# Performance work log

Measured on AMD Instinct MI355X. Metric: run time of the kernel, lower is better.

The kernel has to match this reference:

```python
import jax, jax.numpy as jnp
import numpy as np

N = 20000
E = 640000
D = 128
NORM_FACTOR = 100.0
LN_EPS = 1e-5


def _layer_norm(x, g, b):
    mu = jnp.mean(x, axis=-1, keepdims=True)
    var = jnp.var(x, axis=-1, keepdims=True)
    return (x - mu) * jax.lax.rsqrt(var + LN_EPS) * g + b


def setup_inputs() -> dict:
    key = jax.random.key(0)
    ks = jax.random.split(key, 16)

    def lin(k, fan_in, shape):
        bound = 1.0 / np.sqrt(fan_in)
        return jax.random.uniform(k, shape, jnp.float32, -bound, bound)

    h = jax.random.normal(ks[0], (N, D), jnp.float32)
    distances = jax.random.uniform(ks[1], (E, 1), jnp.float32)
    edges = jax.random.randint(ks[2], (2, E), 0, N, jnp.int64)
    node_mask = jnp.ones((N, 1), jnp.float32)
    edge_mask = jnp.ones((E, 1), jnp.float32)

    return {
        "h": h, "distances": distances, "node_mask": node_mask, "edge_mask": edge_mask,
        # linear: in->out
        "lin_w": lin(ks[3], D, (D, D)), "lin_b": lin(ks[4], D, (D,)),
        # att_mlp: (2D+1)->2D -> 2D->D -> D->1
        "att_w1": lin(ks[5], 2 * D + 1, (2 * D, 2 * D + 1)), "att_b1": lin(ks[5], 2 * D + 1, (2 * D,)),
        "att_w2": lin(ks[6], 2 * D, (D, 2 * D)), "att_b2": lin(ks[6], 2 * D, (D,)),
        "att_w3": lin(ks[7], D, (1, D)), "att_b3": lin(ks[7], D, (1,)),
        # node_mlp: D->D, LN, SiLU, D->D
        "nm_w1": lin(ks[8], D, (D, D)), "nm_b1": lin(ks[8], D, (D,)),
        "nm_ln_g": jnp.ones((D,), jnp.float32), "nm_ln_b": jnp.zeros((D,), jnp.float32),
        "nm_w2": lin(ks[9], D, (D, D)), "nm_b2": lin(ks[9], D, (D,)),
        # final LayerNorm
        "ln_g": jnp.ones((D,), jnp.float32), "ln_b": jnp.zeros((D,), jnp.float32),
        "edges": edges,
    }


def reference(h, distances, node_mask, edge_mask,
              lin_w, lin_b, att_w1, att_b1, att_w2, att_b2, att_w3, att_b3,
              nm_w1, nm_b1, nm_ln_g, nm_ln_b, nm_w2, nm_b2, ln_g, ln_b, edges):
    x = h @ lin_w.T + lin_b                                  # [N, D]
    row, col = edges[0], edges[1]
    x_row = x[row]                                           # [E, D]
    x_col = x[col]                                           # [E, D]

    # DenseAtt
    d = distances * edge_mask
    x_cat = jnp.concatenate([x_row, x_col, d], axis=1)       # [E, 2D+1]
    a = jax.nn.silu(x_cat @ att_w1.T + att_b1)
    a = jax.nn.silu(a @ att_w2.T + att_b2)
    att = jax.nn.sigmoid(a @ att_w3.T + att_b3) * edge_mask  # [E, 1]

    agg = x_col * att                                        # [E, D]
    out = jax.ops.segment_sum(agg, row, num_segments=N) / NORM_FACTOR

    # node_mlp + residual
    o = out @ nm_w1.T + nm_b1
    o = jax.nn.silu(_layer_norm(o, nm_ln_g, nm_ln_b))
    o = o @ nm_w2.T + nm_b2
    hh = o + x

    hh = _layer_norm(hh, ln_g, ln_b)
    hh = jax.nn.silu(hh)                                     # act = SiLU
    return hh
```

## Files before the change

### kernel.cpp

```cpp
#include <hip/hip_runtime.h>
#include <hip/hip_bf16.h>

#define N_NODES 20000
#define E_EDGES 640000
#define DIM 128
#define CAP 96
#define EPB 64
#define NPB 8
#define XST 264

typedef __attribute__((ext_vector_type(8))) short bf16x8;
typedef __attribute__((ext_vector_type(4))) float f32x4;

#define LOG2E 1.44269504f
__device__ __forceinline__ float fsilu(float x) {
    return x * __builtin_amdgcn_rcpf(1.f + __builtin_amdgcn_exp2f(-LOG2E * x));
}
__device__ __forceinline__ float fsig(float x) {
    return __builtin_amdgcn_rcpf(1.f + __builtin_amdgcn_exp2f(-LOG2E * x));
}

__device__ __forceinline__ unsigned short f2bf(float x) {
    union { float f; unsigned u; } v; v.f = x;
    unsigned r = (v.u + 0x7fffu + ((v.u >> 16) & 1u)) >> 16;
    return (unsigned short)r;
}
__device__ __forceinline__ float bf2f(unsigned short s) {
    union { unsigned u; float f; } v; v.u = ((unsigned)s) << 16;
    return v.f;
}
__device__ __forceinline__ unsigned pack_bf16(float lo, float hi) {
    union { float f; unsigned u; } a, b; a.f = lo; b.f = hi;
    unsigned ul = a.u + 0x8000u, uh = b.u + 0x8000u;
    return __builtin_amdgcn_perm(uh, ul, 0x07060302u);
}

#define PRE_PREP_BLOCKS 64
#define PRE_LIN_BLOCKS  625
#define PRE_ADJ_BLOCKS  2500
__global__ __launch_bounds__(256) void pre_kernel(
    const float* __restrict__ w1, const float* __restrict__ w2,
    unsigned short* __restrict__ w1b, float* __restrict__ w1last,
    unsigned short* __restrict__ w2b,
    const float* __restrict__ h, const float* __restrict__ lw,
    const float* __restrict__ lb, float* __restrict__ x,
    unsigned short* __restrict__ xb,
    const int* __restrict__ edges, int* __restrict__ cnt,
    int2* __restrict__ adj2, int E) {
    __shared__ float hs[32][128];
    int b = blockIdx.x;
    int t = threadIdx.x;

    if (b < PRE_PREP_BLOCKS) {
        int i = b * 256 + t;
        const int stride = PRE_PREP_BLOCKS * 256;
        for (int idx = i; idx < 256 * 256; idx += stride) {
            int o = idx >> 8, k = idx & 255;
            w1b[idx] = f2bf(w1[o * 257 + k]);
        }
        for (int idx = i; idx < 128 * 256; idx += stride) {
            int n2 = idx >> 8, p = idx & 255;
            int bb = p & ~31, off = p & 31;
            int ksrc = bb + (off >> 1) + ((off & 1) << 4);
            w2b[idx] = f2bf(w2[n2 * 256 + ksrc]);
        }
        for (int idx = i; idx < 256; idx += stride)
            w1last[idx] = w1[idx * 257 + 256];
    } else if (b < PRE_PREP_BLOCKS + PRE_LIN_BLOCKS) {
        int nb = b - PRE_PREP_BLOCKS;
        int n0 = nb * 32;
        int ch = t & 127, g = t >> 7;
#pragma unroll
        for (int j = 0; j < 16; ++j) hs[g * 16 + j][ch] = h[(size_t)(n0 + g * 16 + j) * DIM + ch];
        __syncthreads();
        float acc[16];
#pragma unroll
        for (int j = 0; j < 16; ++j) acc[j] = 0.f;
        for (int kc = 0; kc < 128; kc += 4) {
            float4 wv = *(const float4*)&lw[(size_t)ch * DIM + kc];
#pragma unroll
            for (int j = 0; j < 16; ++j)
                acc[j] += wv.x * hs[g * 16 + j][kc] + wv.y * hs[g * 16 + j][kc + 1]
                        + wv.z * hs[g * 16 + j][kc + 2] + wv.w * hs[g * 16 + j][kc + 3];
        }
        float bias = lb[ch];
#pragma unroll
        for (int j = 0; j < 16; ++j) {
            float v = acc[j] + bias;
            int n = n0 + g * 16 + j;
            x[(size_t)n * DIM + ch] = v;
            xb[(size_t)n * DIM + ch] = f2bf(v);
        }
    } else {
        int e = (b - PRE_PREP_BLOCKS - PRE_LIN_BLOCKS) * 256 + t;
        if (e < E) {
            int r = edges[e];
            int col = edges[E + e];
            int slot = atomicAdd(&cnt[r], 1);
            if (slot < CAP) { int2 v; v.x = e; v.y = col; adj2[(size_t)r * CAP + slot] = v; }
        }
    }
}

__global__ __launch_bounds__(512, 4) void edge_kernel(
    const unsigned short* __restrict__ xb,
    const float* __restrict__ dist, const float* __restrict__ emask,
    const int* __restrict__ edges,
    const unsigned short* __restrict__ w1b, const float* __restrict__ w1last,
    const float* __restrict__ b1,
    const unsigned short* __restrict__ w2b, const float* __restrict__ b2,
    const float* __restrict__ w3, const float* __restrict__ b3v,
    float* __restrict__ att, int E) {
    __shared__ unsigned short buf[EPB * XST];
    __shared__ float part[8][EPB];
    __shared__ float dvals[EPB];
    __shared__ int ridx[EPB], cidx[EPB];

    int tid = threadIdx.x;
    int eb = blockIdx.x * EPB;

    if (tid < EPB) {
        int e = eb + tid;
        ridx[tid] = edges[e];
        cidx[tid] = edges[E + e];
        dvals[tid] = dist[e] * emask[e];
    }
    __syncthreads();

#pragma unroll
    for (int i = 0; i < 4; ++i) {
        int c = tid + 512 * i;
        int r = c >> 5;
        int cb = (c & 31) * 8;
        const unsigned short* src;
        if (cb < 128) src = xb + (size_t)ridx[r] * DIM + cb;
        else          src = xb + (size_t)cidx[r] * DIM + (cb - 128);
        *(bf16x8*)&buf[r * XST + cb] = *(const bf16x8*)src;
    }

    int wave = tid >> 6, lane = tid & 63;
    int lrow = lane & 15, quad = lane >> 4;
    int nb = wave * 32;

    float bias0 = b1[nb + lrow], bias1 = b1[nb + 16 + lrow];
    float wl0 = w1last[nb + lrow], wl1 = w1last[nb + 16 + lrow];
    int n2 = wave * 16 + lrow;
    float bias2 = b2[n2];
    float w3v = w3[n2];

    __syncthreads();

    f32x4 z = {0.f, 0.f, 0.f, 0.f};
    f32x4 acc1[4][2];
#pragma unroll
    for (int mt = 0; mt < 4; ++mt)
#pragma unroll
        for (int nt = 0; nt < 2; ++nt) acc1[mt][nt] = z;

    for (int kk = 0; kk < 8; ++kk) {
        int ka = kk * 32 + quad * 8;
        bf16x8 a[4];
#pragma unroll
        for (int mt = 0; mt < 4; ++mt)
            a[mt] = *(bf16x8*)&buf[(mt * 16 + lrow) * XST + ka];
#pragma unroll
        for (int nt = 0; nt < 2; ++nt) {
            int n = nb + nt * 16 + lrow;
            bf16x8 bfrag = *(const bf16x8*)&w1b[(size_t)n * 256 + ka];
#pragma unroll
            for (int mt = 0; mt < 4; ++mt)
                acc1[mt][nt] = __builtin_amdgcn_mfma_f32_16x16x32_bf16(a[mt], bfrag, acc1[mt][nt], 0, 0, 0);
        }
    }
    __syncthreads();

    int colbase = nb + 2 * lrow;
#pragma unroll
    for (int mt = 0; mt < 4; ++mt) {
#pragma unroll
        for (int r = 0; r < 4; ++r) {
            int m = mt * 16 + quad * 4 + r;
            float dv = dvals[m];
            float v0 = fsilu(acc1[mt][0][r] + bias0 + dv * wl0);
            float v1 = fsilu(acc1[mt][1][r] + bias1 + dv * wl1);
            *(unsigned*)&buf[m * XST + colbase] = pack_bf16(v0, v1);
        }
    }
    __syncthreads();

    f32x4 acc2[4];
#pragma unroll
    for (int mt = 0; mt < 4; ++mt) acc2[mt] = z;

    for (int kk = 0; kk < 8; ++kk) {
        int ka = kk * 32 + quad * 8;
        bf16x8 bfrag = *(const bf16x8*)&w2b[(size_t)n2 * 256 + ka];
#pragma unroll
        for (int mt = 0; mt < 4; ++mt) {
            bf16x8 a = *(bf16x8*)&buf[(mt * 16 + lrow) * XST + ka];
            acc2[mt] = __builtin_amdgcn_mfma_f32_16x16x32_bf16(a, bfrag, acc2[mt], 0, 0, 0);
        }
    }

    float s[4][4];
#pragma unroll
    for (int mt = 0; mt < 4; ++mt)
#pragma unroll
        for (int r = 0; r < 4; ++r)
            s[mt][r] = fsilu(acc2[mt][r] + bias2) * w3v;
#pragma unroll
    for (int off = 1; off < 16; off <<= 1) {
#pragma unroll
        for (int mt = 0; mt < 4; ++mt)
#pragma unroll
            for (int r = 0; r < 4; ++r)
                s[mt][r] += __shfl_xor(s[mt][r], off);
    }
    if (lrow == 0) {
#pragma unroll
        for (int mt = 0; mt < 4; ++mt)
#pragma unroll
            for (int r = 0; r < 4; ++r)
                part[wave][mt * 16 + quad * 4 + r] = s[mt][r];
    }
    __syncthreads();

    if (tid < EPB) {
        float ssum = b3v[0];
#pragma unroll
        for (int w = 0; w < 8; ++w) ssum += part[w][tid];
        att[eb + tid] = fsig(ssum) * emask[eb + tid];
    }
}

__global__ __launch_bounds__(256) void node_kernel(
    const float* __restrict__ attv, const int2* __restrict__ adj2, const int* __restrict__ cnt,
    const unsigned short* __restrict__ xb,
    const float* __restrict__ x,
    const float* __restrict__ w1, const float* __restrict__ bb1,
    const float* __restrict__ lng, const float* __restrict__ lnb,
    const float* __restrict__ w2, const float* __restrict__ bb2,
    const float* __restrict__ gF, const float* __restrict__ bF,
    float* __restrict__ out, int E) {
    __shared__ float atts[NPB][CAP];
    __shared__ int   cols[NPB][CAP];
    __shared__ float outv[NPB][128];
    __shared__ float bufs[NPB][128];
    __shared__ float mu_s[NPB], rs_s[NPB];
    __shared__ int cnts[NPB];

    int t = threadIdx.x;
    int n0 = blockIdx.x * NPB;

    if (t < NPB) { int c = cnt[n0 + t]; cnts[t] = c > CAP ? CAP : c; }
    __syncthreads();

    {
        int jg = t >> 5, l = t & 31;
        int c = cnts[jg];
        const int2* al = adj2 + (size_t)(n0 + jg) * CAP;
        for (int i = l; i < c; i += 32) {
            int2 v = al[i];
            atts[jg][i] = attv[v.x];
            cols[jg][i] = v.y;
        }
    }
    __syncthreads();

    int w = t >> 6, lane = t & 63;
#pragma unroll
    for (int jj = 0; jj < 2; ++jj) {
        int j = w * 2 + jj;
        int c = cnts[j];
        float lo0 = 0.f, hi0 = 0.f, lo1 = 0.f, hi1 = 0.f;
        float lo2 = 0.f, hi2 = 0.f, lo3 = 0.f, hi3 = 0.f;
        int i = 0;
        for (; i + 3 < c; i += 4) {
            unsigned u0 = *(const unsigned*)&xb[(size_t)cols[j][i]     * DIM + lane * 2];
            unsigned u1 = *(const unsigned*)&xb[(size_t)cols[j][i + 1] * DIM + lane * 2];
            unsigned u2 = *(const unsigned*)&xb[(size_t)cols[j][i + 2] * DIM + lane * 2];
            unsigned u3 = *(const unsigned*)&xb[(size_t)cols[j][i + 3] * DIM + lane * 2];
            float w0 = atts[j][i], w1v = atts[j][i + 1], w2v = atts[j][i + 2], w3v = atts[j][i + 3];
            lo0 += w0 * bf2f((unsigned short)(u0 & 0xffff)); hi0 += w0 * bf2f((unsigned short)(u0 >> 16));
            lo1 += w1v * bf2f((unsigned short)(u1 & 0xffff)); hi1 += w1v * bf2f((unsigned short)(u1 >> 16));
            lo2 += w2v * bf2f((unsigned short)(u2 & 0xffff)); hi2 += w2v * bf2f((unsigned short)(u2 >> 16));
            lo3 += w3v * bf2f((unsigned short)(u3 & 0xffff)); hi3 += w3v * bf2f((unsigned short)(u3 >> 16));
        }
        for (; i < c; ++i) {
            unsigned u0 = *(const unsigned*)&xb[(size_t)cols[j][i] * DIM + lane * 2];
            float w0 = atts[j][i];
            lo0 += w0 * bf2f((unsigned short)(u0 & 0xffff));
            hi0 += w0 * bf2f((unsigned short)(u0 >> 16));
        }
        outv[j][lane * 2]     = ((lo0 + lo1) + (lo2 + lo3)) * 0.01f;
        outv[j][lane * 2 + 1] = ((hi0 + hi1) + (hi2 + hi3)) * 0.01f;
    }
    __syncthreads();

    int h = t >> 7, ch = t & 127;
    float xres[4];
#pragma unroll
    for (int jj = 0; jj < 4; ++jj)
        xres[jj] = x[(size_t)(n0 + h * 4 + jj) * DIM + ch];

    float a1[4] = {0, 0, 0, 0};
    for (int kc = 0; kc < 128; kc += 4) {
        float4 wv = *(const float4*)&w1[(size_t)ch * DIM + kc];
#pragma unroll
        for (int jj = 0; jj < 4; ++jj) {
            int j = h * 4 + jj;
            a1[jj] += wv.x * outv[j][kc] + wv.y * outv[j][kc + 1] + wv.z * outv[j][kc + 2] + wv.w * outv[j][kc + 3];
        }
    }
    float bias1 = bb1[ch];
#pragma unroll
    for (int jj = 0; jj < 4; ++jj) bufs[h * 4 + jj][ch] = a1[jj] + bias1;
    __syncthreads();

    {
        int j = t >> 5, l = t & 31;
        float s = 0.f, qq = 0.f;
#pragma unroll
        for (int i = 0; i < 4; ++i) { float v = bufs[j][l + 32 * i]; s += v; qq += v * v; }
#pragma unroll
        for (int off = 16; off; off >>= 1) { s += __shfl_xor(s, off); qq += __shfl_xor(qq, off); }
        if (l == 0) {
            float mu = s * (1.f / 128.f);
            float var = qq * (1.f / 128.f) - mu * mu;
            mu_s[j] = mu; rs_s[j] = __builtin_amdgcn_rsqf(var + 1e-5f);
        }
    }
    __syncthreads();

    float g = lng[ch], bb = lnb[ch];
    float h2[4];
#pragma unroll
    for (int jj = 0; jj < 4; ++jj) {
        int j = h * 4 + jj;
        h2[jj] = fsilu((bufs[j][ch] - mu_s[j]) * rs_s[j] * g + bb);
    }
    __syncthreads();
#pragma unroll
    for (int jj = 0; jj < 4; ++jj) bufs[h * 4 + jj][ch] = h2[jj];
    __syncthreads();

    float a3[4] = {0, 0, 0, 0};
    for (int kc = 0; kc < 128; kc += 4) {
        float4 wv = *(const float4*)&w2[(size_t)ch * DIM + kc];
#pragma unroll
        for (int jj = 0; jj < 4; ++jj) {
            int j = h * 4 + jj;
            a3[jj] += wv.x * bufs[j][kc] + wv.y * bufs[j][kc + 1] + wv.z * bufs[j][kc + 2] + wv.w * bufs[j][kc + 3];
        }
    }
    float bias2 = bb2[ch];
    float hh[4];
#pragma unroll
    for (int jj = 0; jj < 4; ++jj) hh[jj] = a3[jj] + bias2 + xres[jj];
    __syncthreads();
#pragma unroll
    for (int jj = 0; jj < 4; ++jj) bufs[h * 4 + jj][ch] = hh[jj];
    __syncthreads();

    {
        int j = t >> 5, l = t & 31;
        float s = 0.f, qq = 0.f;
#pragma unroll
        for (int i = 0; i < 4; ++i) { float v = bufs[j][l + 32 * i]; s += v; qq += v * v; }
#pragma unroll
        for (int off = 16; off; off >>= 1) { s += __shfl_xor(s, off); qq += __shfl_xor(qq, off); }
        if (l == 0) {
            float mu = s * (1.f / 128.f);
            float var = qq * (1.f / 128.f) - mu * mu;
            mu_s[j] = mu; rs_s[j] = __builtin_amdgcn_rsqf(var + 1e-5f);
        }
    }
    __syncthreads();

    float gf = gF[ch], bf = bF[ch];
#pragma unroll
    for (int jj = 0; jj < 4; ++jj) {
        int j = h * 4 + jj;
        float y = (hh[jj] - mu_s[j]) * rs_s[j] * gf + bf;
        out[(size_t)(n0 + j) * DIM + ch] = fsilu(y);
    }
}

extern "C" void kernel_launch(void* const* d_in, const int* in_sizes, int n_in,
                              void* d_out, int out_size, void* d_ws, size_t ws_size,
                              hipStream_t stream) {
    const float* h         = (const float*)d_in[0];
    const float* distances = (const float*)d_in[1];
    const float* edge_mask = (const float*)d_in[3];
    const float* lin_w     = (const float*)d_in[4];
    const float* lin_b     = (const float*)d_in[5];
    const float* att_w1    = (const float*)d_in[6];
    const float* att_b1    = (const float*)d_in[7];
    const float* att_w2    = (const float*)d_in[8];
    const float* att_b2    = (const float*)d_in[9];
    const float* att_w3    = (const float*)d_in[10];
    const float* att_b3    = (const float*)d_in[11];
    const float* nm_w1     = (const float*)d_in[12];
    const float* nm_b1     = (const float*)d_in[13];
    const float* nm_ln_g   = (const float*)d_in[14];
    const float* nm_ln_b   = (const float*)d_in[15];
    const float* nm_w2     = (const float*)d_in[16];
    const float* nm_b2     = (const float*)d_in[17];
    const float* ln_g      = (const float*)d_in[18];
    const float* ln_b      = (const float*)d_in[19];
    const int*   edges     = (const int*)d_in[20];
    float* out = (float*)d_out;

    const int N = N_NODES, E = E_EDGES;

    char* ws = (char*)d_ws;
    float* x            = (float*)ws;            ws += (size_t)N * DIM * 4;
    unsigned short* xb  = (unsigned short*)ws;   ws += (size_t)N * DIM * 2;
    float* attv         = (float*)ws;            ws += (size_t)E * 4;
    int* cnt            = (int*)ws;              ws += (size_t)N * 4;
    int2* adj2          = (int2*)ws;             ws += (size_t)N * CAP * 8;
    unsigned short* w1b = (unsigned short*)ws;   ws += 256 * 256 * 2;
    float* w1last       = (float*)ws;            ws += 256 * 4;
    unsigned short* w2b = (unsigned short*)ws;   ws += 128 * 256 * 2;

    hipMemsetAsync(cnt, 0, (size_t)N * 4, stream);

    pre_kernel<<<PRE_PREP_BLOCKS + PRE_LIN_BLOCKS + PRE_ADJ_BLOCKS, 256, 0, stream>>>(
        att_w1, att_w2, w1b, w1last, w2b,
        h, lin_w, lin_b, x, xb,
        edges, cnt, adj2, E);
    edge_kernel<<<E / EPB, 512, 0, stream>>>(xb, distances, edge_mask, edges,
                                             w1b, w1last, att_b1, w2b, att_b2,
                                             att_w3, att_b3, attv, E);
    node_kernel<<<N / NPB, 256, 0, stream>>>(attv, adj2, cnt, xb, x,
                                             nm_w1, nm_b1, nm_ln_g, nm_ln_b,
                                             nm_w2, nm_b2, ln_g, ln_b, out, E);
}
```

Before: 490.7 us.

## Precompute per-node first attention layer projections instead of per-edge GEMM

Splits the first attention MLP layer W1·[x_row,x_col,d] into per-node projections P_row=W1a·x+b1 and P_col=W1b·x, computed once per node in a new kernel. The edge kernel then gathers the two 256-wide bf16 projection rows per edge, adds them plus the distance term, and applies SiLU, removing the largest per-edge MFMA GEMM. This trades E×256×256 FLOPs for N×256×256 plus twice-as-wide gathers (512 bf16 values per edge instead of 256). It adds an extra bf16 rounding of the projections before summation and extra workspace.

```diff
diff --git a/kernel.cpp b/kernel.cpp
--- a/kernel.cpp
+++ b/kernel.cpp
@@ -40,7 +40,7 @@
 #define PRE_ADJ_BLOCKS  2500
 __global__ __launch_bounds__(256) void pre_kernel(
     const float* __restrict__ w1, const float* __restrict__ w2,
-    unsigned short* __restrict__ w1b, float* __restrict__ w1last,
+    unsigned short* __restrict__ w1b, float* __restrict__ w1p,
     unsigned short* __restrict__ w2b,
     const float* __restrict__ h, const float* __restrict__ lw,
     const float* __restrict__ lb, float* __restrict__ x,
@@ -64,8 +64,11 @@
             int ksrc = bb + (off >> 1) + ((off & 1) << 4);
             w2b[idx] = f2bf(w2[n2 * 256 + ksrc]);
         }
-        for (int idx = i; idx < 256; idx += stride)
-            w1last[idx] = w1[idx * 257 + 256];
+        for (int idx = i; idx < 256; idx += stride) {
+            int bb = idx & ~31, off = idx & 31;
+            int ksrc = bb + (off >> 1) + ((off & 1) << 4);
+            w1p[idx] = w1[ksrc * 257 + 256];
+        }
     } else if (b < PRE_PREP_BLOCKS + PRE_LIN_BLOCKS) {
         int nb = b - PRE_PREP_BLOCKS;
         int n0 = nb * 32;
@@ -102,17 +105,53 @@
     }
 }
 
+#define PRC_NPB 16
+__global__ __launch_bounds__(256) void prc_kernel(
+    const unsigned short* __restrict__ xb,
+    const unsigned short* __restrict__ w1b,
+    const float* __restrict__ b1,
+    unsigned short* __restrict__ pr, unsigned short* __restrict__ pc) {
+    int n0 = blockIdx.x * PRC_NPB;
+    int w = threadIdx.x >> 6, lane = threadIdx.x & 63;
+    int lrow = lane & 15, quad = lane >> 4;
+
+    bf16x8 a[4];
+#pragma unroll
+    for (int kk = 0; kk < 4; ++kk)
+        a[kk] = *(const bf16x8*)&xb[(size_t)(n0 + lrow) * DIM + kk * 32 + quad * 8];
+
+    f32x4 z = {0.f, 0.f, 0.f, 0.f};
+#pragma unroll
+    for (int i = 0; i < 8; ++i) {
+        int gt = w * 8 + i;
+        int half = gt >> 4;
+        int obase = (gt & 15) * 16;
+        f32x4 acc = z;
+#pragma unroll
+        for (int kk = 0; kk < 4; ++kk) {
+            bf16x8 bfrag = *(const bf16x8*)&w1b[(size_t)(obase + lrow) * 256 + half * 128 + kk * 32 + quad * 8];
+            acc = __builtin_amdgcn_mfma_f32_16x16x32_bf16(a[kk], bfrag, acc, 0, 0, 0);
+        }
+        int o = obase + lrow;
+        float bias = half ? 0.f : b1[o];
+        unsigned short* dst = half ? pc : pr;
+#pragma unroll
+        for (int r = 0; r < 4; ++r)
+            dst[(size_t)(n0 + quad * 4 + r) * 256 + o] = f2bf(acc[r] + bias);
+    }
+}
+
 __global__ __launch_bounds__(512, 4) void edge_kernel(
-    const unsigned short* __restrict__ xb,
+    const unsigned short* __restrict__ pr, const unsigned short* __restrict__ pc,
     const float* __restrict__ dist, const float* __restrict__ emask,
     const int* __restrict__ edges,
-    const unsigned short* __restrict__ w1b, const float* __restrict__ w1last,
-    const float* __restrict__ b1,
+    const float* __restrict__ w1p,
     const unsigned short* __restrict__ w2b, const float* __restrict__ b2,
     const float* __restrict__ w3, const float* __restrict__ b3v,
     float* __restrict__ att, int E) {
     __shared__ unsigned short buf[EPB * XST];
     __shared__ float part[8][EPB];
+    __shared__ float w1ps[256];
     __shared__ float dvals[EPB];
     __shared__ int ridx[EPB], cidx[EPB];
 
@@ -125,72 +164,51 @@
         cidx[tid] = edges[E + e];
         dvals[tid] = dist[e] * emask[e];
     }
-    __syncthreads();
-
-#pragma unroll
-    for (int i = 0; i < 4; ++i) {
-        int c = tid + 512 * i;
-        int r = c >> 5;
-        int cb = (c & 31) * 8;
-        const unsigned short* src;
-        if (cb < 128) src = xb + (size_t)ridx[r] * DIM + cb;
-        else          src = xb + (size_t)cidx[r] * DIM + (cb - 128);
-        *(bf16x8*)&buf[r * XST + cb] = *(const bf16x8*)src;
-    }
+    if (tid >= 64 && tid < 320) w1ps[tid - 64] = w1p[tid - 64];
 
     int wave = tid >> 6, lane = tid & 63;
     int lrow = lane & 15, quad = lane >> 4;
-    int nb = wave * 32;
-
-    float bias0 = b1[nb + lrow], bias1 = b1[nb + 16 + lrow];
-    float wl0 = w1last[nb + lrow], wl1 = w1last[nb + 16 + lrow];
     int n2 = wave * 16 + lrow;
     float bias2 = b2[n2];
     float w3v = w3[n2];
 
     __syncthreads();
 
-    f32x4 z = {0.f, 0.f, 0.f, 0.f};
-    f32x4 acc1[4][2];
-#pragma unroll
-    for (int mt = 0; mt < 4; ++mt)
-#pragma unroll
-        for (int nt = 0; nt < 2; ++nt) acc1[mt][nt] = z;
-
-    for (int kk = 0; kk < 8; ++kk) {
-        int ka = kk * 32 + quad * 8;
-        bf16x8 a[4];
-#pragma unroll
-        for (int mt = 0; mt < 4; ++mt)
-            a[mt] = *(bf16x8*)&buf[(mt * 16 + lrow) * XST + ka];
-#pragma unroll
-        for (int nt = 0; nt < 2; ++nt) {
-            int n = nb + nt * 16 + lrow;
-            bf16x8 bfrag = *(const bf16x8*)&w1b[(size_t)n * 256 + ka];
-#pragma unroll
-            for (int mt = 0; mt < 4; ++mt)
-                acc1[mt][nt] = __builtin_amdgcn_mfma_f32_16x16x32_bf16(a[mt], bfrag, acc1[mt][nt], 0, 0, 0);
-        }
-    }
-    __syncthreads();
-
-    int colbase = nb + 2 * lrow;
-#pragma unroll
-    for (int mt = 0; mt < 4; ++mt) {
-#pragma unroll
-        for (int r = 0; r < 4; ++r) {
-            int m = mt * 16 + quad * 4 + r;
-            float dv = dvals[m];
-            float v0 = fsilu(acc1[mt][0][r] + bias0 + dv * wl0);
-            float v1 = fsilu(acc1[mt][1][r] + bias1 + dv * wl1);
-            *(unsigned*)&buf[m * XST + colbase] = pack_bf16(v0, v1);
-        }
-    }
-    __syncthreads();
-
+    {
+        int ge = tid >> 3, cb = tid & 7;
+        size_t rbase = (size_t)ridx[ge] * 256 + cb * 32;
+        size_t cbase = (size_t)cidx[ge] * 256 + cb * 32;
+        float d = dvals[ge];
+        unsigned* wrow = (unsigned*)&buf[ge * XST + cb * 32];
+        const float* wp = &w1ps[cb * 32];
+
+        bf16x8 pA = *(const bf16x8*)&pr[rbase];
+        bf16x8 pB = *(const bf16x8*)&pr[rbase + 16];
+        bf16x8 qA = *(const bf16x8*)&pc[cbase];
+        bf16x8 qB = *(const bf16x8*)&pc[cbase + 16];
+#pragma unroll
+        for (int l = 0; l < 8; ++l) {
+            float s0 = bf2f((unsigned short)pA[l]) + bf2f((unsigned short)qA[l]) + d * wp[2 * l];
+            float s1 = bf2f((unsigned short)pB[l]) + bf2f((unsigned short)qB[l]) + d * wp[2 * l + 1];
+            wrow[l] = pack_bf16(fsilu(s0), fsilu(s1));
+        }
+        pA = *(const bf16x8*)&pr[rbase + 8];
+        pB = *(const bf16x8*)&pr[rbase + 24];
+        qA = *(const bf16x8*)&pc[cbase + 8];
+        qB = *(const bf16x8*)&pc[cbase + 24];
+#pragma unroll
+        for (int l = 0; l < 8; ++l) {
+            float s0 = bf2f((unsigned short)pA[l]) + bf2f((unsigned short)qA[l]) + d * wp[16 + 2 * l];
+            float s1 = bf2f((unsigned short)pB[l]) + bf2f((unsigned short)qB[l]) + d * wp[16 + 2 * l + 1];
+            wrow[8 + l] = pack_bf16(fsilu(s0), fsilu(s1));
+        }
+    }
+    __syncthreads();
+
+    f32x4 zz = {0.f, 0.f, 0.f, 0.f};
     f32x4 acc2[4];
 #pragma unroll
-    for (int mt = 0; mt < 4; ++mt) acc2[mt] = z;
+    for (int mt = 0; mt < 4; ++mt) acc2[mt] = zz;
 
     for (int kk = 0; kk < 8; ++kk) {
         int ka = kk * 32 + quad * 8;
@@ -420,17 +438,20 @@
     int* cnt            = (int*)ws;              ws += (size_t)N * 4;
     int2* adj2          = (int2*)ws;             ws += (size_t)N * CAP * 8;
     unsigned short* w1b = (unsigned short*)ws;   ws += 256 * 256 * 2;
-    float* w1last       = (float*)ws;            ws += 256 * 4;
+    float* w1p          = (float*)ws;            ws += 256 * 4;
     unsigned short* w2b = (unsigned short*)ws;   ws += 128 * 256 * 2;
+    unsigned short* pr  = (unsigned short*)ws;   ws += (size_t)N * 256 * 2;
+    unsigned short* pc  = (unsigned short*)ws;   ws += (size_t)N * 256 * 2;
 
     hipMemsetAsync(cnt, 0, (size_t)N * 4, stream);
 
     pre_kernel<<<PRE_PREP_BLOCKS + PRE_LIN_BLOCKS + PRE_ADJ_BLOCKS, 256, 0, stream>>>(
-        att_w1, att_w2, w1b, w1last, w2b,
+        att_w1, att_w2, w1b, w1p, w2b,
         h, lin_w, lin_b, x, xb,
         edges, cnt, adj2, E);
-    edge_kernel<<<E / EPB, 512, 0, stream>>>(xb, distances, edge_mask, edges,
-                                             w1b, w1last, att_b1, w2b, att_b2,
+    prc_kernel<<<N / PRC_NPB, 256, 0, stream>>>(xb, w1b, att_b1, pr, pc);
+    edge_kernel<<<E / EPB, 512, 0, stream>>>(pr, pc, distances, edge_mask, edges,
+                                             w1p, w2b, att_b2,
                                              att_w3, att_b3, attv, E);
     node_kernel<<<N / NPB, 256, 0, stream>>>(attv, adj2, cnt, xb, x,
                                              nm_w1, nm_b1, nm_ln_g, nm_ln_b,
```

Result: faster. 398.9 us (-18.7%).
